# Kernel optimization log

Hardware: AMD Instinct MI355X
Metric: run time of the kernel (lower is better)

The kernel has to match this reference:

```python
import jax, jax.numpy as jnp
import numpy as np
from jax import lax

H = 192; W = 192; C = 256; N = H * W; E = 294912; K = 289; DSIG = 1
SLOPE = 0.01
EPS = 1e-5


def leaky(x):
    return jnp.where(x >= 0, x, SLOPE * x)


def conv2d(x, w, pad, groups):
    return lax.conv_general_dilated(
        x, w, (1, 1), [(pad, pad), (pad, pad)],
        dimension_numbers=('NCHW', 'OIHW', 'NCHW'),
        feature_group_count=groups)


def bn2d(x, g, b):
    # BatchNorm2d with track_running_stats=False -> always batch stats (biased var)
    m = x.mean(axis=(0, 2, 3), keepdims=True)
    v = x.var(axis=(0, 2, 3), keepdims=True)
    return (x - m) / jnp.sqrt(v + EPS) * g.reshape(1, -1, 1, 1) + b.reshape(1, -1, 1, 1)


def conv_batch(x, w, g, b, pad, groups):
    # nn.Sequential(LeakyReLU(0.01), Conv2d(bias=False), BatchNorm2d)
    return bn2d(conv2d(leaky(x), w, pad, groups), g, b)


def bn1d(x, g, b):
    m = x.mean(axis=0)
    v = x.var(axis=0)
    return (x - m) / jnp.sqrt(v + EPS) * g + b


def setup_inputs() -> dict:
    key = jax.random.key(0)
    ks = jax.random.split(key, 20)
    X = jax.random.normal(ks[0], (N, C), dtype=jnp.float32)
    src = jax.random.randint(ks[1], (E,), 0, N)
    dst = jax.random.randint(ks[2], (E,), 0, N)
    k1 = jax.random.randint(ks[3], (E,), 0, K)
    k2 = jax.random.randint(ks[4], (E,), 0, K)
    InfoIdx = jnp.stack([src, k1, dst, k2], axis=1).astype(jnp.int64)
    edgmsk = (jax.random.uniform(ks[5], (E, 1)) < 0.9).astype(jnp.float32)
    s = 0.05
    inp = {
        'X': X, 'InfoIdx': InfoIdx, 'edgmsk': edgmsk,
        # PPM: depthwise 17x17 conv_batch then 1x1 conv_batch
        'ppm_w0': jax.random.normal(ks[6], (C, 1, 17, 17), jnp.float32) * s,
        'ppm_g0': jnp.ones((C,), jnp.float32), 'ppm_b0': jnp.zeros((C,), jnp.float32),
        'ppm_w1': jax.random.normal(ks[7], (C, C, 1, 1), jnp.float32) * s,
        'ppm_g1': jnp.ones((C,), jnp.float32), 'ppm_b1': jnp.zeros((C,), jnp.float32),
        # FFN_1: two 1x1 conv_batch
        'ffn1_w0': jax.random.normal(ks[8], (C, C, 1, 1), jnp.float32) * s,
        'ffn1_g0': jnp.ones((C,), jnp.float32), 'ffn1_b0': jnp.zeros((C,), jnp.float32),
        'ffn1_w1': jax.random.normal(ks[9], (C, C, 1, 1), jnp.float32) * s,
        'ffn1_g1': jnp.ones((C,), jnp.float32), 'ffn1_b1': jnp.zeros((C,), jnp.float32),
        # Dis: Linear(C,C) -> LeakyReLU -> Linear(C, 289)
        'dis_w1': jax.random.normal(ks[10], (C, C), jnp.float32) * s,
        'dis_b1': jnp.zeros((C,), jnp.float32),
        'dis_w2': jax.random.normal(ks[11], (K * DSIG, C), jnp.float32) * s,
        'dis_b2': jnp.zeros((K * DSIG,), jnp.float32),
        # BatchNorm1d
        'bn_g': jnp.ones((C,), jnp.float32), 'bn_b': jnp.zeros((C,), jnp.float32),
        # FFN_2 = DoubleConv: depthwise-expand 3x3 (groups=C, out=4C) then 1x1
        'ffn2_w0': jax.random.normal(ks[12], (4 * C, 1, 3, 3), jnp.float32) * s,
        'ffn2_g0': jnp.ones((4 * C,), jnp.float32), 'ffn2_b0': jnp.zeros((4 * C,), jnp.float32),
        'ffn2_w1': jax.random.normal(ks[13], (C, 4 * C, 1, 1), jnp.float32) * s,
        'ffn2_g1': jnp.ones((C,), jnp.float32), 'ffn2_b1': jnp.zeros((C,), jnp.float32),
    }
    return inp


def reference(X, InfoIdx, edgmsk,
              ppm_w0, ppm_g0, ppm_b0, ppm_w1, ppm_g1, ppm_b1,
              ffn1_w0, ffn1_g0, ffn1_b0, ffn1_w1, ffn1_g1, ffn1_b1,
              dis_w1, dis_b1, dis_w2, dis_b2, bn_g, bn_b,
              ffn2_w0, ffn2_g0, ffn2_b0, ffn2_w1, ffn2_g1, ffn2_b1):
    src_idx = InfoIdx[:, 0]
    dst_idx = InfoIdx[:, 2]
    # [N,C] -> [1,C,H,W]
    img = X.T.reshape(1, C, H, W)
    # PPM residual
    t = conv_batch(img, ppm_w0, ppm_g0, ppm_b0, pad=8, groups=C)
    t = conv_batch(t, ppm_w1, ppm_g1, ppm_b1, pad=0, groups=1)
    img = img + t
    # FFN_1 residual
    t = conv_batch(img, ffn1_w0, ffn1_g0, ffn1_b0, pad=0, groups=1)
    t = conv_batch(t, ffn1_w1, ffn1_g1, ffn1_b1, pad=0, groups=1)
    img = img + t
    Xn = img.reshape(C, N).T  # [N, C]
    # Dis MLP -> signal [N, 289, d_signal]
    h = leaky(Xn @ dis_w1.T + dis_b1)
    signal = (h @ dis_w2.T + dis_b2).reshape(N, K, DSIG)
    # edge gather + exp/clamp score
    s_src = signal[src_idx, InfoIdx[:, 1]]  # [E, 1]
    s_dst = signal[dst_idx, InfoIdx[:, 3]]  # [E, 1]
    aij = jnp.exp(jnp.clip(s_src + s_dst, -5.0, 5.0)) * edgmsk  # [E, 1]
    # two scatter-sum reductions to dst nodes
    A_sum = jax.ops.segment_sum(aij, dst_idx, num_segments=N)  # [N, 1]
    XA_sum = jax.ops.segment_sum(Xn[src_idx] * aij, dst_idx, num_segments=N)  # [N, C]
    X_trans = XA_sum / (A_sum + 1e-5)
    Xn = Xn + bn1d(X_trans, bn_g, bn_b)
    # FFN_2 = DoubleConv with residual skip
    img = Xn.T.reshape(1, C, H, W)
    t = conv_batch(img, ffn2_w0, ffn2_g0, ffn2_b0, pad=1, groups=C)
    t = conv_batch(t, ffn2_w1, ffn2_g1, ffn2_b1, pad=0, groups=1)
    out = t + img
    return out.reshape(C, N).T  # final bg.ndata['X'], [N, C]
```

## Files before the change

kernel.cpp:

```cpp
#include <hip/hip_runtime.h>
#include <cstddef>

#define HW 192
#define NP 36864
#define CH 256
#define EDGES 294912
#define KSIG 289
#define SLOPE 0.01f
#define BNEPS 1e-5f
#define PADW 208
#define PADSZ (PADW * PADW)
#define NP32 ((size_t)NP * 32)

typedef unsigned short u16;
typedef __attribute__((ext_vector_type(8))) short bf16x8;
typedef __attribute__((ext_vector_type(4))) float f32x4;

__device__ __forceinline__ float leaky(float x) { return x >= 0.f ? x : SLOPE * x; }
__device__ __forceinline__ u16 f2bf(float x) {
  unsigned u = __float_as_uint(x);
  unsigned r = (u + 0x7fffu + ((u >> 16) & 1u)) >> 16;
  return (u16)r;
}
__device__ __forceinline__ float bf2f(unsigned h) { return __uint_as_float(h << 16); }
__device__ __forceinline__ void bnss(const float* sums, const float* sqs,
                                     const float* g, const float* b, int k,
                                     float& s, float& h) {
  float mean = sums[k] * (1.f / NP);
  float var = sqs[k] * (1.f / NP) - mean * mean;
  s = g[k] * rsqrtf(var + BNEPS);
  h = b[k] - mean * s;
}

__global__ __launch_bounds__(256) void k_transpose_pad(const float* __restrict__ src,
                                                       float* __restrict__ dst,
                                                       u16* __restrict__ pad) {
  __shared__ float tile[32][33];
  int s0 = blockIdx.x * 32, r0 = blockIdx.y * 32;
  int tx = threadIdx.x & 31, ty = threadIdx.x >> 5;
#pragma unroll
  for (int j = 0; j < 4; j++)
    tile[ty + 8 * j][tx] = src[(size_t)(r0 + ty + 8 * j) * CH + s0 + tx];
  __syncthreads();
  int n = r0 + tx;
  int y = n / HW, x = n - y * HW;
#pragma unroll
  for (int j = 0; j < 4; j++) {
    int c = s0 + ty + 8 * j;
    float v = tile[tx][ty + 8 * j];
    dst[(size_t)c * NP + n] = v;
    pad[(size_t)c * PADSZ + (y + 8) * PADW + x + 8] = f2bf(leaky(v));
  }
}

__global__ __launch_bounds__(256) void k_mkT(const float* __restrict__ w,
                                             u16* __restrict__ Tg) {
  int c = blockIdx.x;
  const float* wc = w + c * 289;
  u16* tc = Tg + (size_t)c * 8704;
  for (int i = threadIdx.x; i < 8704; i += 256) {
    int ky = i >> 9, rem = i & 511, n = rem >> 5, k = rem & 31;
    int kx = k - n;
    float v = (kx >= 0 && kx < 17) ? wc[ky * 17 + kx] : 0.f;
    tc[i] = f2bf(v);
  }
}

__global__ __launch_bounds__(256) void k_cvtW(const float* __restrict__ pw1,
                                              const float* __restrict__ f1w0,
                                              const float* __restrict__ f1w1,
                                              const float* __restrict__ dw1,
                                              const float* __restrict__ dw2,
                                              const float* __restrict__ f2w1,
                                              u16* __restrict__ out) {
  int i = blockIdx.x * 256 + threadIdx.x;
  float v;
  int off, j, R, Klog;
  if (i < 65536)       { off = 0;      j = i;          v = pw1[j];  R = 256; Klog = 8; }
  else if (i < 131072) { off = 65536;  j = i - 65536;  v = f1w0[j]; R = 256; Klog = 8; }
  else if (i < 196608) { off = 131072; j = i - 131072; v = f1w1[j]; R = 256; Klog = 8; }
  else if (i < 262144) { off = 196608; j = i - 196608; v = dw1[j];  R = 256; Klog = 8; }
  else if (i < 360448) { off = 262144; j = i - 262144;
                         v = (j < KSIG * 256) ? dw2[j] : 0.f;       R = 384; Klog = 8; }
  else                 { off = 360448; j = i - 360448; v = f2w1[j]; R = 256; Klog = 10; }
  int r = j >> Klog, k = j & ((1 << Klog) - 1);
  int ni = off + (k >> 5) * (R * 32) + r * 32 + (k & 31);
  out[ni] = f2bf(v);
}

__global__ __launch_bounds__(256) void k_stats_bf(const u16* __restrict__ Xr,
                                                  float* __restrict__ sums,
                                                  float* __restrict__ sqs) {
  int row = blockIdx.x;
  int t = threadIdx.x;
  const uint4* p = (const uint4*)(Xr + (size_t)row * NP);
  float s = 0.f, q = 0.f;
  for (int i = t; i < NP / 8; i += 256) {
    uint4 v = p[i];
    unsigned w[4] = {v.x, v.y, v.z, v.w};
#pragma unroll
    for (int j = 0; j < 4; j++) {
      float a = bf2f(w[j] & 0xffffu), c = bf2f(w[j] >> 16);
      s += a + c; q += a * a + c * c;
    }
  }
  __shared__ float ss[256], qq[256];
  ss[t] = s; qq[t] = q;
  __syncthreads();
  for (int d = 128; d > 0; d >>= 1) {
    if (t < d) { ss[t] += ss[t + d]; qq[t] += qq[t + d]; }
    __syncthreads();
  }
  if (t == 0) { sums[row] = ss[0]; sqs[row] = qq[0]; }
}

__global__ __launch_bounds__(256) void k_cvtT(const float* __restrict__ in,
                                              u16* __restrict__ outT, int M) {
  __shared__ float tile[32][65];
  int n0 = blockIdx.x * 64, k0 = blockIdx.y * 32;
  int t = threadIdx.x;
#pragma unroll
  for (int i = 0; i < 2; i++) {
    int ci = i * 256 + t;
    int k = ci >> 4, cg = (ci & 15) * 4;
    float4 v = *(const float4*)&in[(size_t)(k0 + k) * NP + n0 + cg];
    tile[k][cg] = v.x; tile[k][cg + 1] = v.y; tile[k][cg + 2] = v.z; tile[k][cg + 3] = v.w;
  }
  __syncthreads();
  int n = t >> 2, kg = (t & 3) * 8;
  uint4 o;
  o.x = (unsigned)f2bf(tile[kg + 0][n]) | ((unsigned)f2bf(tile[kg + 1][n]) << 16);
  o.y = (unsigned)f2bf(tile[kg + 2][n]) | ((unsigned)f2bf(tile[kg + 3][n]) << 16);
  o.z = (unsigned)f2bf(tile[kg + 4][n]) | ((unsigned)f2bf(tile[kg + 5][n]) << 16);
  o.w = (unsigned)f2bf(tile[kg + 6][n]) | ((unsigned)f2bf(tile[kg + 7][n]) << 16);
  *(uint4*)&outT[(size_t)(k0 >> 5) * NP32 + (size_t)(n0 + n) * 32 + kg] = o;
}

__global__ __launch_bounds__(256) void k_cvtT_bf(const u16* __restrict__ in,
                                                 u16* __restrict__ outT,
                                                 const float* __restrict__ sums,
                                                 const float* __restrict__ sqs,
                                                 const float* __restrict__ g,
                                                 const float* __restrict__ b, int M) {
  __shared__ float tile[32][65];
  int n0 = blockIdx.x * 64, k0 = blockIdx.y * 32;
  int t = threadIdx.x;
  int k = t >> 3, cg = (t & 7) * 8;
  float s, h; bnss(sums, sqs, g, b, k0 + k, s, h);
  uint4 v = *(const uint4*)&in[(size_t)(k0 + k) * NP + n0 + cg];
  unsigned w[4] = {v.x, v.y, v.z, v.w};
#pragma unroll
  for (int j = 0; j < 4; j++) {
    tile[k][cg + 2 * j]     = leaky(fmaf(bf2f(w[j] & 0xffffu), s, h));
    tile[k][cg + 2 * j + 1] = leaky(fmaf(bf2f(w[j] >> 16), s, h));
  }
  __syncthreads();
  int n = t >> 2, kg = (t & 3) * 8;
  uint4 o;
  o.x = (unsigned)f2bf(tile[kg + 0][n]) | ((unsigned)f2bf(tile[kg + 1][n]) << 16);
  o.y = (unsigned)f2bf(tile[kg + 2][n]) | ((unsigned)f2bf(tile[kg + 3][n]) << 16);
  o.z = (unsigned)f2bf(tile[kg + 4][n]) | ((unsigned)f2bf(tile[kg + 5][n]) << 16);
  o.w = (unsigned)f2bf(tile[kg + 6][n]) | ((unsigned)f2bf(tile[kg + 7][n]) << 16);
  *(uint4*)&outT[(size_t)(k0 >> 5) * NP32 + (size_t)(n0 + n) * 32 + kg] = o;
}

__global__ __launch_bounds__(256) void k_fuse1(const float* __restrict__ base,
                                               const u16* __restrict__ raw,
                                               const float* __restrict__ sums,
                                               const float* __restrict__ sqs,
                                               const float* __restrict__ g,
                                               const float* __restrict__ b,
                                               float* __restrict__ img2,
                                               u16* __restrict__ outT) {
  __shared__ float tile[32][65];
  int n0 = blockIdx.x * 64, k0 = blockIdx.y * 32;
  int t = threadIdx.x;
#pragma unroll
  for (int i = 0; i < 2; i++) {
    int ci = i * 256 + t;
    int k = ci >> 4, cg = (ci & 15) * 4;
    float s, h; bnss(sums, sqs, g, b, k0 + k, s, h);
    size_t idx = (size_t)(k0 + k) * NP + n0 + cg;
    float4 bv = *(const float4*)&base[idx];
    uint2 rv = *(const uint2*)&raw[idx];
    float r0 = bf2f(rv.x & 0xffffu), r1 = bf2f(rv.x >> 16);
    float r2 = bf2f(rv.y & 0xffffu), r3 = bf2f(rv.y >> 16);
    float4 o;
    o.x = bv.x + fmaf(r0, s, h); o.y = bv.y + fmaf(r1, s, h);
    o.z = bv.z + fmaf(r2, s, h); o.w = bv.w + fmaf(r3, s, h);
    *(float4*)&img2[idx] = o;
    tile[k][cg]     = leaky(o.x);
    tile[k][cg + 1] = leaky(o.y);
    tile[k][cg + 2] = leaky(o.z);
    tile[k][cg + 3] = leaky(o.w);
  }
  __syncthreads();
  int n = t >> 2, kg = (t & 3) * 8;
  uint4 o;
  o.x = (unsigned)f2bf(tile[kg + 0][n]) | ((unsigned)f2bf(tile[kg + 1][n]) << 16);
  o.y = (unsigned)f2bf(tile[kg + 2][n]) | ((unsigned)f2bf(tile[kg + 3][n]) << 16);
  o.z = (unsigned)f2bf(tile[kg + 4][n]) | ((unsigned)f2bf(tile[kg + 5][n]) << 16);
  o.w = (unsigned)f2bf(tile[kg + 6][n]) | ((unsigned)f2bf(tile[kg + 7][n]) << 16);
  *(uint4*)&outT[(size_t)(k0 >> 5) * NP32 + (size_t)(n0 + n) * 32 + kg] = o;
}

__global__ __launch_bounds__(256) void k_fuse2(const float* __restrict__ base,
                                               const u16* __restrict__ raw,
                                               const float* __restrict__ sums,
                                               const float* __restrict__ sqs,
                                               const float* __restrict__ g,
                                               const float* __restrict__ b,
                                               float* __restrict__ XnT,
                                               u16* __restrict__ outT,
                                               u16* __restrict__ outTt) {
  __shared__ float tile[32][65];
  int n0 = blockIdx.x * 64, k0 = blockIdx.y * 32;
  int t = threadIdx.x;
#pragma unroll
  for (int i = 0; i < 2; i++) {
    int ci = i * 256 + t;
    int k = ci >> 4, cg = (ci & 15) * 4;
    float s, h; bnss(sums, sqs, g, b, k0 + k, s, h);
    size_t idx = (size_t)(k0 + k) * NP + n0 + cg;
    float4 bv = *(const float4*)&base[idx];
    uint2 rv = *(const uint2*)&raw[idx];
    float r0 = bf2f(rv.x & 0xffffu), r1 = bf2f(rv.x >> 16);
    float r2 = bf2f(rv.y & 0xffffu), r3 = bf2f(rv.y >> 16);
    tile[k][cg]     = bv.x + fmaf(r0, s, h);
    tile[k][cg + 1] = bv.y + fmaf(r1, s, h);
    tile[k][cg + 2] = bv.z + fmaf(r2, s, h);
    tile[k][cg + 3] = bv.w + fmaf(r3, s, h);
  }
  __syncthreads();
  int n = t >> 2, kg = (t & 3) * 8;
  float4 f0 = {tile[kg + 0][n], tile[kg + 1][n], tile[kg + 2][n], tile[kg + 3][n]};
  float4 f1 = {tile[kg + 4][n], tile[kg + 5][n], tile[kg + 6][n], tile[kg + 7][n]};
  *(float4*)&XnT[(size_t)(n0 + n) * CH + k0 + kg] = f0;
  *(float4*)&XnT[(size_t)(n0 + n) * CH + k0 + kg + 4] = f1;
  uint4 o;
  o.x = (unsigned)f2bf(f0.x) | ((unsigned)f2bf(f0.y) << 16);
  o.y = (unsigned)f2bf(f0.z) | ((unsigned)f2bf(f0.w) << 16);
  o.z = (unsigned)f2bf(f1.x) | ((unsigned)f2bf(f1.y) << 16);
  o.w = (unsigned)f2bf(f1.z) | ((unsigned)f2bf(f1.w) << 16);
  *(uint4*)&outT[(size_t)(n0 + n) * CH + k0 + kg] = o;
  *(uint4*)&outTt[(size_t)(k0 >> 5) * NP32 + (size_t)(n0 + n) * 32 + kg] = o;
}

__global__ __launch_bounds__(256) void k_mgemm(const u16* __restrict__ A,
                                               const u16* __restrict__ Bt,
                                               float* __restrict__ Outf,
                                               u16* __restrict__ Outb,
                                               const float* __restrict__ bias,
                                               int K, int Mstore, int actout,
                                               int aslab) {
  __shared__ u16 As[128 * 40];
  __shared__ u16 Bs[128 * 40];
  int t = threadIdx.x;
  int lane = t & 63, wave = t >> 6;
  int wm = (wave >> 1) * 64, wn = (wave & 1) * 64;
  int m0 = blockIdx.y * 128, n0 = blockIdx.x * 128;
  int r = lane & 15, q = lane >> 4;
  f32x4 acc[4][4];
#pragma unroll
  for (int a = 0; a < 4; a++)
#pragma unroll
    for (int b = 0; b < 4; b++) acc[a][b] = (f32x4){0.f, 0.f, 0.f, 0.f};

  for (int k0 = 0; k0 < K; k0 += 32) {
    size_t ab = (size_t)(k0 >> 5) * aslab + (size_t)m0 * 32;
    size_t bb = (size_t)(k0 >> 5) * NP32 + (size_t)n0 * 32;
#pragma unroll
    for (int i = 0; i < 2; i++) {
      int cc = t + i * 256;
      int mm = cc >> 2, kq = (cc & 3) * 8;
      uint4 av = *(const uint4*)&A[ab + (size_t)cc * 8];
      uint4 bv = *(const uint4*)&Bt[bb + (size_t)cc * 8];
      *(uint4*)&As[mm * 40 + kq] = av;
      *(uint4*)&Bs[mm * 40 + kq] = bv;
    }
    __syncthreads();
    bf16x8 af[4], bfr[4];
#pragma unroll
    for (int mt = 0; mt < 4; mt++)
      af[mt] = *(const bf16x8*)&As[(wm + mt * 16 + r) * 40 + q * 8];
#pragma unroll
    for (int nt = 0; nt < 4; nt++)
      bfr[nt] = *(const bf16x8*)&Bs[(wn + nt * 16 + r) * 40 + q * 8];
#pragma unroll
    for (int mt = 0; mt < 4; mt++)
#pragma unroll
      for (int nt = 0; nt < 4; nt++)
        acc[mt][nt] = __builtin_amdgcn_mfma_f32_16x16x32_bf16(af[mt], bfr[nt], acc[mt][nt], 0, 0, 0);
    __syncthreads();
  }
#pragma unroll
  for (int mt = 0; mt < 4; mt++) {
    int mrow = m0 + wm + mt * 16 + q * 4;
#pragma unroll
    for (int i = 0; i < 4; i++) {
      int m = mrow + i;
      if (m >= Mstore) continue;
      float bs = bias ? bias[m] : 0.f;
#pragma unroll
      for (int nt = 0; nt < 4; nt++) {
        float v = acc[mt][nt][i] + bs;
        if (actout) v = leaky(v);
        size_t oi = (size_t)m * NP + n0 + wn + nt * 16 + r;
        if (Outb) Outb[oi] = f2bf(v); else Outf[oi] = v;
      }
    }
  }
}

__global__ __launch_bounds__(512) void k_mgemm256(const u16* __restrict__ A,
                                                  const u16* __restrict__ Bt,
                                                  float* __restrict__ Outf,
                                                  u16* __restrict__ Outb,
                                                  const float* __restrict__ bias,
                                                  int K, int actout) {
  __shared__ u16 As[256 * 40];
  __shared__ u16 Bs[128 * 40];
  int t = threadIdx.x;
  int lane = t & 63, wave = t >> 6;
  int wm = (wave >> 1) * 64, wn = (wave & 1) * 64;
  int n0 = blockIdx.x * 128;
  int r = lane & 15, q = lane >> 4;
  int arow0 = t >> 2, kq = (t & 3) * 8;
  f32x4 acc[4][4];
#pragma unroll
  for (int a = 0; a < 4; a++)
#pragma unroll
    for (int b = 0; b < 4; b++) acc[a][b] = (f32x4){0.f, 0.f, 0.f, 0.f};

  uint4 pa0, pa1, pb;
  pa0 = *(const uint4*)&A[(size_t)t * 8];
  pa1 = *(const uint4*)&A[4096 + (size_t)t * 8];
  pb  = *(const uint4*)&Bt[(size_t)n0 * 32 + (size_t)t * 8];
  int kiters = K >> 5;
  for (int ki = 0; ki < kiters; ki++) {
    *(uint4*)&As[arow0 * 40 + kq] = pa0;
    *(uint4*)&As[(arow0 + 128) * 40 + kq] = pa1;
    *(uint4*)&Bs[arow0 * 40 + kq] = pb;
    __syncthreads();
    if (ki + 1 < kiters) {
      size_t ab = (size_t)(ki + 1) * 8192;
      size_t bb = (size_t)(ki + 1) * NP32 + (size_t)n0 * 32;
      pa0 = *(const uint4*)&A[ab + (size_t)t * 8];
      pa1 = *(const uint4*)&A[ab + 4096 + (size_t)t * 8];
      pb  = *(const uint4*)&Bt[bb + (size_t)t * 8];
    }
    bf16x8 af[4], bfr[4];
#pragma unroll
    for (int mt = 0; mt < 4; mt++)
      af[mt] = *(const bf16x8*)&As[(wm + mt * 16 + r) * 40 + q * 8];
#pragma unroll
    for (int nt = 0; nt < 4; nt++)
      bfr[nt] = *(const bf16x8*)&Bs[(wn + nt * 16 + r) * 40 + q * 8];
#pragma unroll
    for (int mt = 0; mt < 4; mt++)
#pragma unroll
      for (int nt = 0; nt < 4; nt++)
        acc[mt][nt] = __builtin_amdgcn_mfma_f32_16x16x32_bf16(af[mt], bfr[nt], acc[mt][nt], 0, 0, 0);
    __syncthreads();
  }
#pragma unroll
  for (int mt = 0; mt < 4; mt++) {
    int mrow = wm + mt * 16 + q * 4;
#pragma unroll
    for (int i = 0; i < 4; i++) {
      int m = mrow + i;
      float bs = bias ? bias[m] : 0.f;
#pragma unroll
      for (int nt = 0; nt < 4; nt++) {
        float v = acc[mt][nt][i] + bs;
        if (actout) v = leaky(v);
        size_t oi = (size_t)m * NP + n0 + wn + nt * 16 + r;
        if (Outb) Outb[oi] = f2bf(v); else Outf[oi] = v;
      }
    }
  }
}

__global__ __launch_bounds__(256) void k_dwconv17(const u16* __restrict__ pad,
                                                  const u16* __restrict__ Tg,
                                                  u16* __restrict__ outb) {
  int c = blockIdx.y;
  int tile = blockIdx.x;
  int ty0 = (tile / 3) * 64, tx0 = (tile % 3) * 64;
  __shared__ u16 smIn[80 * 88];
  __shared__ u16 smT[17 * 16 * 40];
  const u16* pc = pad + (size_t)c * PADSZ;
  for (int cc = threadIdx.x; cc < 800; cc += 256) {
    int rr = cc / 10, j = cc - rr * 10;
    uint4 v = *(const uint4*)(pc + (ty0 + rr) * PADW + tx0 + j * 8);
    *(uint4*)(smIn + rr * 88 + j * 8) = v;
  }
  const u16* tc = Tg + (size_t)c * 8704;
  for (int cc = threadIdx.x; cc < 1088; cc += 256) {
    int rr = cc >> 2, j = cc & 3;
    uint4 v = *(const uint4*)(tc + rr * 32 + j * 8);
    *(uint4*)(smT + rr * 40 + j * 8) = v;
  }
  __syncthreads();
  int lane = threadIdx.x & 63, wave = threadIdx.x >> 6;
  int wy = wave * 16;
  int r = lane & 15, q = lane >> 4;
  f32x4 acc[4];
#pragma unroll
  for (int xt = 0; xt < 4; xt++) acc[xt] = (f32x4){0.f, 0.f, 0.f, 0.f};
#pragma unroll
  for (int ky = 0; ky < 17; ky++) {
    bf16x8 bfrag = *(const bf16x8*)&smT[(ky * 16 + r) * 40 + q * 8];
    int rowA = wy + r + ky;
#pragma unroll
    for (int xt = 0; xt < 4; xt++) {
      bf16x8 afrag = *(const bf16x8*)&smIn[rowA * 88 + xt * 16 + q * 8];
      acc[xt] = __builtin_amdgcn_mfma_f32_16x16x32_bf16(afrag, bfrag, acc[xt], 0, 0, 0);
    }
  }
  u16* oc = outb + (size_t)c * NP;
#pragma unroll
  for (int xt = 0; xt < 4; xt++) {
    int x = tx0 + xt * 16 + r;
#pragma unroll
    for (int i = 0; i < 4; i++) {
      int y = ty0 + wy + q * 4 + i;
      oc[y * HW + x] = f2bf(acc[xt][i]);
    }
  }
}

__global__ __launch_bounds__(256) void k_conv3x4(const float* __restrict__ in,
                                                 const float* __restrict__ w,
                                                 u16* __restrict__ out) {
  int wave = threadIdx.x >> 6, lane = threadIdx.x & 63;
  int c = blockIdx.y;
  int y = blockIdx.x * 4 + wave;
  const float* wc = w + (size_t)(4 * c) * 9;
  float wr[36];
#pragma unroll
  for (int k = 0; k < 36; k++) wr[k] = wc[k];
  float acc[4][3];
#pragma unroll
  for (int oc = 0; oc < 4; oc++)
#pragma unroll
    for (int s = 0; s < 3; s++) acc[oc][s] = 0.f;
  const float* base = in + (size_t)c * NP;
#pragma unroll
  for (int ky = 0; ky < 3; ky++) {
    int ry = y + ky - 1;
    if (ry < 0 || ry >= HW) continue;
    const float* rp = base + ry * HW;
    float a0 = leaky(rp[lane]);
    float a1 = leaky(rp[64 + lane]);
    float a2 = leaky(rp[128 + lane]);
    float e0 = __shfl(a0, 63), e1 = __shfl(a1, 63);
    float b1 = __shfl(a1, 0),  b2 = __shfl(a2, 0);
    float l0 = __shfl_up(a0, 1); if (lane == 0) l0 = 0.f;
    float l1 = __shfl_up(a1, 1); if (lane == 0) l1 = e0;
    float l2 = __shfl_up(a2, 1); if (lane == 0) l2 = e1;
    float r0 = __shfl_down(a0, 1); if (lane == 63) r0 = b1;
    float r1 = __shfl_down(a1, 1); if (lane == 63) r1 = b2;
    float r2 = __shfl_down(a2, 1); if (lane == 63) r2 = 0.f;
#pragma unroll
    for (int oc = 0; oc < 4; oc++) {
      float w0 = wr[oc * 9 + ky * 3], w1 = wr[oc * 9 + ky * 3 + 1], w2 = wr[oc * 9 + ky * 3 + 2];
      acc[oc][0] = fmaf(w0, l0, fmaf(w1, a0, fmaf(w2, r0, acc[oc][0])));
      acc[oc][1] = fmaf(w0, l1, fmaf(w1, a1, fmaf(w2, r1, acc[oc][1])));
      acc[oc][2] = fmaf(w0, l2, fmaf(w1, a2, fmaf(w2, r2, acc[oc][2])));
    }
  }
  size_t ob = (size_t)(4 * c) * NP + (size_t)y * HW + lane;
#pragma unroll
  for (int oc = 0; oc < 4; oc++) {
    out[ob + (size_t)oc * NP]       = f2bf(acc[oc][0]);
    out[ob + (size_t)oc * NP + 64]  = f2bf(acc[oc][1]);
    out[ob + (size_t)oc * NP + 128] = f2bf(acc[oc][2]);
  }
}

__global__ __launch_bounds__(256) void k_edge(const int* __restrict__ info,
                                              const float* __restrict__ msk,
                                              const float* __restrict__ sig,
                                              float* __restrict__ aij,
                                              int* __restrict__ counts) {
  int e = blockIdx.x * 256 + threadIdx.x;
  int4 ii = ((const int4*)info)[e];
  float s = sig[(size_t)ii.y * NP + ii.x] + sig[(size_t)ii.w * NP + ii.z];
  s = fminf(fmaxf(s, -5.f), 5.f);
  aij[e] = expf(s) * msk[e];
  atomicAdd(&counts[ii.z], 1);
}

__global__ __launch_bounds__(256) void k_scan1(const int* __restrict__ counts,
                                               int* __restrict__ offsets,
                                               int* __restrict__ bsum) {
  __shared__ int sm[256];
  int t = threadIdx.x;
  int i = blockIdx.x * 256 + t;
  int v = counts[i];
  sm[t] = v;
  __syncthreads();
  for (int d = 1; d < 256; d <<= 1) {
    int add = (t >= d) ? sm[t - d] : 0;
    __syncthreads();
    sm[t] += add;
    __syncthreads();
  }
  offsets[i] = sm[t] - v;
  if (t == 255) bsum[blockIdx.x] = sm[255];
}
__global__ __launch_bounds__(256) void k_scan2(const int* __restrict__ bsum,
                                               int* __restrict__ boff) {
  __shared__ int sm[256];
  int t = threadIdx.x;
  int v = (t < 144) ? bsum[t] : 0;
  sm[t] = v;
  __syncthreads();
  for (int d = 1; d < 256; d <<= 1) {
    int add = (t >= d) ? sm[t - d] : 0;
    __syncthreads();
    sm[t] += add;
    __syncthreads();
  }
  boff[t] = sm[t] - v;
}
__global__ __launch_bounds__(256) void k_scan3(int* __restrict__ offsets,
                                               const int* __restrict__ boff,
                                               int* __restrict__ cursor) {
  int i = blockIdx.x * 256 + threadIdx.x;
  int o = offsets[i] + boff[blockIdx.x];
  offsets[i] = o;
  cursor[i] = o;
  if (i == 0) offsets[NP] = EDGES;
}
__global__ __launch_bounds__(256) void k_scatter(const int* __restrict__ info,
                                                 const float* __restrict__ aij,
                                                 int* __restrict__ cursor,
                                                 int* __restrict__ srcs,
                                                 float* __restrict__ aijw) {
  int e = blockIdx.x * 256 + threadIdx.x;
  int4 ii = ((const int4*)info)[e];
  int pos = atomicAdd(&cursor[ii.z], 1);
  srcs[pos] = ii.x;
  aijw[pos] = aij[e];
}

__global__ __launch_bounds__(256) void k_agg(const int* __restrict__ offsets,
                                             const int* __restrict__ srcs,
                                             const float* __restrict__ aijw,
                                             const u16* __restrict__ XnBf,
                                             u16* __restrict__ XtrBf) {
  int wave = threadIdx.x >> 6, lane = threadIdx.x & 63;
  int node = blockIdx.x * 4 + wave;
  int o0 = offsets[node], o1 = offsets[node + 1];
  int half = lane >> 5, l32 = lane & 31;
  float acc[8] = {0.f, 0.f, 0.f, 0.f, 0.f, 0.f, 0.f, 0.f};
  float asum = 0.f;
  int i = o0 + half;
  for (; i + 2 < o1; i += 4) {
    int s0 = srcs[i], s1 = srcs[i + 2];
    float a0 = aijw[i], a1 = aijw[i + 2];
    uint4 v0 = ((const uint4*)(XnBf + (size_t)s0 * CH))[l32];
    uint4 v1 = ((const uint4*)(XnBf + (size_t)s1 * CH))[l32];
    unsigned w0[4] = {v0.x, v0.y, v0.z, v0.w};
    unsigned w1[4] = {v1.x, v1.y, v1.z, v1.w};
#pragma unroll
    for (int j = 0; j < 4; j++) {
      acc[2 * j]     = fmaf(a0, bf2f(w0[j] & 0xffffu), acc[2 * j]);
      acc[2 * j + 1] = fmaf(a0, bf2f(w0[j] >> 16),     acc[2 * j + 1]);
      acc[2 * j]     = fmaf(a1, bf2f(w1[j] & 0xffffu), acc[2 * j]);
      acc[2 * j + 1] = fmaf(a1, bf2f(w1[j] >> 16),     acc[2 * j + 1]);
    }
    asum += a0 + a1;
  }
  for (; i < o1; i += 2) {
    int s = srcs[i];
    float a = aijw[i];
    uint4 v = ((const uint4*)(XnBf + (size_t)s * CH))[l32];
    unsigned w[4] = {v.x, v.y, v.z, v.w};
#pragma unroll
    for (int j = 0; j < 4; j++) {
      acc[2 * j]     = fmaf(a, bf2f(w[j] & 0xffffu), acc[2 * j]);
      acc[2 * j + 1] = fmaf(a, bf2f(w[j] >> 16),     acc[2 * j + 1]);
    }
    asum += a;
  }
#pragma unroll
  for (int j = 0; j < 8; j++) acc[j] += __shfl_xor(acc[j], 32, 64);
  asum += __shfl_xor(asum, 32, 64);
  if (half == 0) {
    float inv = 1.f / (asum + 1e-5f);
    uint4 o;
    o.x = (unsigned)f2bf(acc[0] * inv) | ((unsigned)f2bf(acc[1] * inv) << 16);
    o.y = (unsigned)f2bf(acc[2] * inv) | ((unsigned)f2bf(acc[3] * inv) << 16);
    o.z = (unsigned)f2bf(acc[4] * inv) | ((unsigned)f2bf(acc[5] * inv) << 16);
    o.w = (unsigned)f2bf(acc[6] * inv) | ((unsigned)f2bf(acc[7] * inv) << 16);
    ((uint4*)(XtrBf + (size_t)node * CH))[l32] = o;
  }
}

__global__ __launch_bounds__(256) void k_colstats(const u16* __restrict__ Xt,
                                                  float* __restrict__ sums,
                                                  float* __restrict__ sqs) {
  int c = threadIdx.x;
  float s = 0.f, q = 0.f;
  for (int n = blockIdx.x; n < NP; n += gridDim.x) {
    float v = bf2f(Xt[(size_t)n * CH + c]);
    s += v; q += v * v;
  }
  atomicAdd(&sums[c], s);
  atomicAdd(&sqs[c], q);
}

__global__ __launch_bounds__(256) void k_mkimg4(const float* __restrict__ Xn,
                                                const u16* __restrict__ XtrBf,
                                                const float* __restrict__ sums,
                                                const float* __restrict__ sqs,
                                                const float* __restrict__ g,
                                                const float* __restrict__ b,
                                                float* __restrict__ img4) {
  __shared__ float tile[32][33];
  int c0 = blockIdx.x * 32, n0 = blockIdx.y * 32;
  int tx = threadIdx.x & 31, ty = threadIdx.x >> 5;
  int c = c0 + tx;
  float s, h; bnss(sums, sqs, g, b, c, s, h);
#pragma unroll
  for (int j = 0; j < 4; j++) {
    size_t idx = (size_t)(n0 + ty + 8 * j) * CH + c;
    tile[ty + 8 * j][tx] = Xn[idx] + fmaf(bf2f(XtrBf[idx]), s, h);
  }
  __syncthreads();
#pragma unroll
  for (int j = 0; j < 4; j++) {
    int cc = c0 + ty + 8 * j;
    img4[(size_t)cc * NP + n0 + tx] = tile[tx][ty + 8 * j];
  }
}

__global__ __launch_bounds__(256) void k_final(const u16* __restrict__ raw5,
                                               const float* __restrict__ img4,
                                               const float* __restrict__ sums,
                                               const float* __restrict__ sqs,
                                               const float* __restrict__ g,
                                               const float* __restrict__ b,
                                               float* __restrict__ out) {
  __shared__ float tile[32][33];
  int n0 = blockIdx.x * 32, c0 = blockIdx.y * 32;
  int tx = threadIdx.x & 31, ty = threadIdx.x >> 5;
#pragma unroll
  for (int j = 0; j < 4; j++) {
    int c = c0 + ty + 8 * j;
    float s, h; bnss(sums, sqs, g, b, c, s, h);
    size_t idx = (size_t)c * NP + n0 + tx;
    tile[ty + 8 * j][tx] = fmaf(bf2f(raw5[idx]), s, h) + img4[idx];
  }
  __syncthreads();
#pragma unroll
  for (int j = 0; j < 4; j++) {
    int n = n0 + ty + 8 * j;
    out[(size_t)n * CH + c0 + tx] = tile[tx][ty + 8 * j];
  }
}

extern "C" void kernel_launch(void* const* d_in, const int* in_sizes, int n_in,
                              void* d_out, int out_size, void* d_ws, size_t ws_size,
                              hipStream_t stream) {
  (void)in_sizes; (void)n_in; (void)out_size; (void)ws_size;
  const float* X    = (const float*)d_in[0];
  const int*   info = (const int*)d_in[1];
  const float* msk  = (const float*)d_in[2];
  const float* pw0  = (const float*)d_in[3];
  const float* pg0  = (const float*)d_in[4];
  const float* pb0  = (const float*)d_in[5];
  const float* pw1  = (const float*)d_in[6];
  const float* pg1  = (const float*)d_in[7];
  const float* pb1  = (const float*)d_in[8];
  const float* f1w0 = (const float*)d_in[9];
  const float* f1g0 = (const float*)d_in[10];
  const float* f1b0 = (const float*)d_in[11];
  const float* f1w1 = (const float*)d_in[12];
  const float* f1g1 = (const float*)d_in[13];
  const float* f1b1 = (const float*)d_in[14];
  const float* dw1  = (const float*)d_in[15];
  const float* db1  = (const float*)d_in[16];
  const float* dw2  = (const float*)d_in[17];
  const float* db2  = (const float*)d_in[18];
  const float* bng  = (const float*)d_in[19];
  const float* bnb  = (const float*)d_in[20];
  const float* f2w0 = (const float*)d_in[21];
  const float* f2g0 = (const float*)d_in[22];
  const float* f2b0 = (const float*)d_in[23];
  const float* f2w1 = (const float*)d_in[24];
  const float* f2g1 = (const float*)d_in[25];
  const float* f2b1 = (const float*)d_in[26];
  float* out = (float*)d_out;

  float* ws = (float*)d_ws;
  float* sum0 = ws + 0;    float* sq0 = ws + 256;
  float* sum1 = ws + 512;  float* sq1 = ws + 768;
  float* sum2 = ws + 1024; float* sq2 = ws + 1280;
  float* sum3 = ws + 1536; float* sq3 = ws + 1792;
  float* sum5 = ws + 2048; float* sq5 = ws + 2304;
  float* sumT = ws + 2560; float* sqT = ws + 2816;
  float* sum4 = ws + 3072; float* sq4 = ws + 4096;
  int* counts  = (int*)(ws + 8192);
  int* offsets = (int*)(ws + 45056);
  int* cursor  = (int*)(ws + 82176);
  int* bsum    = (int*)(ws + 119296);
  int* boff    = (int*)(ws + 119552);
  int* srcs    = (int*)(ws + 131072);
  float* aij   = ws + 425984;
  const size_t S = (size_t)NP * CH;
  float* slotD = ws + 720896;
  float* slotB = slotD + S;
  float* slotA = slotB + S;
  float* slotC = slotA + S;
  u16* bfB  = (u16*)(slotC + S);
  u16* bfH  = bfB + S;
  float* sigT = (float*)(bfH + S);
  u16* bfW  = (u16*)(sigT + (size_t)KSIG * NP);
  float* aijw = (float*)(bfW + 622592);
  u16* Ppad = (u16*)slotC;
  u16* Tg   = (u16*)slotD;
  u16* raw4bf  = (u16*)slotB;
  u16* bfT1024 = bfB;
  u16* XtrBf   = (u16*)slotD;
  u16* raw5bf  = (u16*)slotB;
  u16* bfBt    = (u16*)sigT;

  hipMemsetAsync(ws, 0, 5120 * sizeof(float), stream);
  hipMemsetAsync(counts, 0, NP * sizeof(int), stream);
  hipMemsetAsync(Ppad, 0, (size_t)PADSZ * CH * sizeof(u16), stream);

  dim3 b256(256), b512(512);
  k_cvtW<<<2432, b256, 0, stream>>>(pw1, f1w0, f1w1, dw1, dw2, f2w1, bfW);
  k_mkT<<<CH, b256, 0, stream>>>(pw0, Tg);
  k_transpose_pad<<<dim3(CH / 32, NP / 32), b256, 0, stream>>>(X, slotA, Ppad);
  k_dwconv17<<<dim3(9, CH), b256, 0, stream>>>(Ppad, Tg, bfH);
  k_stats_bf<<<CH, b256, 0, stream>>>(bfH, sum0, sq0);
  k_cvtT_bf<<<dim3(NP / 64, 8), b256, 0, stream>>>(bfH, bfB, sum0, sq0, pg0, pb0, CH);
  k_mgemm256<<<NP / 128, b512, 0, stream>>>(bfW, bfB, nullptr, bfH, nullptr, CH, 0);
  k_stats_bf<<<CH, b256, 0, stream>>>(bfH, sum1, sq1);
  k_fuse1<<<dim3(NP / 64, 8), b256, 0, stream>>>(slotA, bfH, sum1, sq1, pg1, pb1, slotD, bfB);
  k_mgemm256<<<NP / 128, b512, 0, stream>>>(bfW + 65536, bfB, nullptr, bfH, nullptr, CH, 0);
  k_stats_bf<<<CH, b256, 0, stream>>>(bfH, sum2, sq2);
  k_cvtT_bf<<<dim3(NP / 64, 8), b256, 0, stream>>>(bfH, bfB, sum2, sq2, f1g0, f1b0, CH);
  k_mgemm256<<<NP / 128, b512, 0, stream>>>(bfW + 131072, bfB, nullptr, bfH, nullptr, CH, 0);
  k_stats_bf<<<CH, b256, 0, stream>>>(bfH, sum3, sq3);
  k_fuse2<<<dim3(NP / 64, 8), b256, 0, stream>>>(slotD, bfH, sum3, sq3, f1g1, f1b1, slotA, bfB, bfBt);
  k_mgemm256<<<NP / 128, b512, 0, stream>>>(bfW + 196608, bfBt, slotC, nullptr, db1, CH, 1);
  k_cvtT<<<dim3(NP / 64, 8), b256, 0, stream>>>(slotC, bfH, CH);
  k_mgemm<<<dim3(NP / 128, 3), b256, 0, stream>>>(bfW + 262144, bfH, sigT, nullptr, db2, CH, KSIG, 0, 12288);
  k_edge<<<EDGES / 256, b256, 0, stream>>>(info, msk, sigT, aij, counts);
  k_scan1<<<NP / 256, b256, 0, stream>>>(counts, offsets, bsum);
  k_scan2<<<1, b256, 0, stream>>>(bsum, boff);
  k_scan3<<<NP / 256, b256, 0, stream>>>(offsets, boff, cursor);
  k_scatter<<<EDGES / 256, b256, 0, stream>>>(info, aij, cursor, srcs, aijw);
  k_agg<<<NP / 4, b256, 0, stream>>>(offsets, srcs, aijw, bfB, XtrBf);
  k_colstats<<<288, b256, 0, stream>>>(XtrBf, sumT, sqT);
  k_mkimg4<<<dim3(CH / 32, NP / 32), b256, 0, stream>>>(slotA, XtrBf, sumT, sqT, bng, bnb, slotC);
  k_conv3x4<<<dim3(48, CH), b256, 0, stream>>>(slotC, f2w0, raw4bf);
  k_stats_bf<<<1024, b256, 0, stream>>>(raw4bf, sum4, sq4);
  k_cvtT_bf<<<dim3(NP / 64, 32), b256, 0, stream>>>(raw4bf, bfT1024, sum4, sq4, f2g0, f2b0, 1024);
  k_mgemm256<<<NP / 128, b512, 0, stream>>>(bfW + 360448, bfT1024, nullptr, raw5bf, nullptr, 1024, 0);
  k_stats_bf<<<CH, b256, 0, stream>>>(raw5bf, sum5, sq5);
  k_final<<<dim3(NP / 32, CH / 32), b256, 0, stream>>>(raw5bf, slotC, sum5, sq5, f2g1, f2b1, out);
}
```

Before: 642.6 us.

## Load MFMA operands directly from global memory, dropping LDS staging in GEMMs

Both bf16 MFMA GEMM kernels no longer stage A and B tiles through shared memory. Each lane now reads its bf16x8 fragments straight from the slab-packed global layout, and the __syncthreads barriers go away. This removes LDS write/read traffic and block-wide synchronisation. In exchange, every operand is fetched redundantly by multiple waves through L1/L2, and the register prefetch pipeline in the 256-row kernel is lost.

```diff
diff --git a/kernel.cpp b/kernel.cpp
--- a/kernel.cpp
+++ b/kernel.cpp
@@ -253,45 +253,33 @@
                                                const float* __restrict__ bias,
                                                int K, int Mstore, int actout,
                                                int aslab) {
-  __shared__ u16 As[128 * 40];
-  __shared__ u16 Bs[128 * 40];
   int t = threadIdx.x;
   int lane = t & 63, wave = t >> 6;
   int wm = (wave >> 1) * 64, wn = (wave & 1) * 64;
   int m0 = blockIdx.y * 128, n0 = blockIdx.x * 128;
   int r = lane & 15, q = lane >> 4;
+  const u16* Ab = A + (size_t)(m0 + wm + r) * 32 + q * 8;
+  const u16* Bb = Bt + (size_t)(n0 + wn + r) * 32 + q * 8;
   f32x4 acc[4][4];
 #pragma unroll
   for (int a = 0; a < 4; a++)
 #pragma unroll
     for (int b = 0; b < 4; b++) acc[a][b] = (f32x4){0.f, 0.f, 0.f, 0.f};
 
-  for (int k0 = 0; k0 < K; k0 += 32) {
-    size_t ab = (size_t)(k0 >> 5) * aslab + (size_t)m0 * 32;
-    size_t bb = (size_t)(k0 >> 5) * NP32 + (size_t)n0 * 32;
-#pragma unroll
-    for (int i = 0; i < 2; i++) {
-      int cc = t + i * 256;
-      int mm = cc >> 2, kq = (cc & 3) * 8;
-      uint4 av = *(const uint4*)&A[ab + (size_t)cc * 8];
-      uint4 bv = *(const uint4*)&Bt[bb + (size_t)cc * 8];
-      *(uint4*)&As[mm * 40 + kq] = av;
-      *(uint4*)&Bs[mm * 40 + kq] = bv;
-    }
-    __syncthreads();
+  int kiters = K >> 5;
+  for (int ki = 0; ki < kiters; ki++) {
+    const u16* Ap = Ab + (size_t)ki * aslab;
+    const u16* Bp = Bb + (size_t)ki * NP32;
     bf16x8 af[4], bfr[4];
 #pragma unroll
-    for (int mt = 0; mt < 4; mt++)
-      af[mt] = *(const bf16x8*)&As[(wm + mt * 16 + r) * 40 + q * 8];
-#pragma unroll
-    for (int nt = 0; nt < 4; nt++)
-      bfr[nt] = *(const bf16x8*)&Bs[(wn + nt * 16 + r) * 40 + q * 8];
+    for (int mt = 0; mt < 4; mt++) af[mt] = *(const bf16x8*)(Ap + mt * 512);
+#pragma unroll
+    for (int nt = 0; nt < 4; nt++) bfr[nt] = *(const bf16x8*)(Bp + nt * 512);
 #pragma unroll
     for (int mt = 0; mt < 4; mt++)
 #pragma unroll
       for (int nt = 0; nt < 4; nt++)
         acc[mt][nt] = __builtin_amdgcn_mfma_f32_16x16x32_bf16(af[mt], bfr[nt], acc[mt][nt], 0, 0, 0);
-    __syncthreads();
   }
 #pragma unroll
   for (int mt = 0; mt < 4; mt++) {
@@ -318,50 +306,33 @@
                                                   u16* __restrict__ Outb,
                                                   const float* __restrict__ bias,
                                                   int K, int actout) {
-  __shared__ u16 As[256 * 40];
-  __shared__ u16 Bs[128 * 40];
   int t = threadIdx.x;
   int lane = t & 63, wave = t >> 6;
   int wm = (wave >> 1) * 64, wn = (wave & 1) * 64;
   int n0 = blockIdx.x * 128;
   int r = lane & 15, q = lane >> 4;
-  int arow0 = t >> 2, kq = (t & 3) * 8;
+  const u16* Ab = A + (size_t)(wm + r) * 32 + q * 8;
+  const u16* Bb = Bt + (size_t)(n0 + wn + r) * 32 + q * 8;
   f32x4 acc[4][4];
 #pragma unroll
   for (int a = 0; a < 4; a++)
 #pragma unroll
     for (int b = 0; b < 4; b++) acc[a][b] = (f32x4){0.f, 0.f, 0.f, 0.f};
 
-  uint4 pa0, pa1, pb;
-  pa0 = *(const uint4*)&A[(size_t)t * 8];
-  pa1 = *(const uint4*)&A[4096 + (size_t)t * 8];
-  pb  = *(const uint4*)&Bt[(size_t)n0 * 32 + (size_t)t * 8];
   int kiters = K >> 5;
   for (int ki = 0; ki < kiters; ki++) {
-    *(uint4*)&As[arow0 * 40 + kq] = pa0;
-    *(uint4*)&As[(arow0 + 128) * 40 + kq] = pa1;
-    *(uint4*)&Bs[arow0 * 40 + kq] = pb;
-    __syncthreads();
-    if (ki + 1 < kiters) {
-      size_t ab = (size_t)(ki + 1) * 8192;
-      size_t bb = (size_t)(ki + 1) * NP32 + (size_t)n0 * 32;
-      pa0 = *(const uint4*)&A[ab + (size_t)t * 8];
-      pa1 = *(const uint4*)&A[ab + 4096 + (size_t)t * 8];
-      pb  = *(const uint4*)&Bt[bb + (size_t)t * 8];
-    }
+    const u16* Ap = Ab + (size_t)ki * 8192;
+    const u16* Bp = Bb + (size_t)ki * NP32;
     bf16x8 af[4], bfr[4];
 #pragma unroll
-    for (int mt = 0; mt < 4; mt++)
-      af[mt] = *(const bf16x8*)&As[(wm + mt * 16 + r) * 40 + q * 8];
-#pragma unroll
-    for (int nt = 0; nt < 4; nt++)
-      bfr[nt] = *(const bf16x8*)&Bs[(wn + nt * 16 + r) * 40 + q * 8];
+    for (int mt = 0; mt < 4; mt++) af[mt] = *(const bf16x8*)(Ap + mt * 512);
+#pragma unroll
+    for (int nt = 0; nt < 4; nt++) bfr[nt] = *(const bf16x8*)(Bp + nt * 512);
 #pragma unroll
     for (int mt = 0; mt < 4; mt++)
 #pragma unroll
       for (int nt = 0; nt < 4; nt++)
         acc[mt][nt] = __builtin_amdgcn_mfma_f32_16x16x32_bf16(af[mt], bfr[nt], acc[mt][nt], 0, 0, 0);
-    __syncthreads();
   }
 #pragma unroll
   for (int mt = 0; mt < 4; mt++) {
```

Measured after the change: 689.6 us. +7.3%, slower.
